# Optimization experiments

Measured on AMD Instinct MI355X. Metric: run time of the kernel, lower is better.

The kernel has to match this reference:

```python
import jax, jax.numpy as jnp
import numpy as np

B, P, D = 64, 1024, 768

def setup_inputs() -> dict:
    key = jax.random.key(0)
    k1, k2, k3 = jax.random.split(key, 3)
    z = jax.random.normal(k1, (B, P, D), dtype=jnp.float32)
    q = jax.random.normal(k2, (1, 1, D), dtype=jnp.float32)
    W_proj = jax.random.normal(k3, (D, D), dtype=jnp.float32) * (1.0 / np.sqrt(D))
    return {"z": z, "q": q, "W_proj": W_proj}

def reference(z, q, W_proj):
    # k = Linear(z) with weight W_proj (torch: z @ W.T), no bias
    k = jnp.einsum("bpd,ed->bpe", z, W_proj)          # [B,P,D]
    d = z.shape[-1]
    scale = 1.0 / jnp.sqrt(jnp.asarray(d, dtype=z.dtype))
    # single learnable query broadcast over batch: scores [B,1,P]
    scores = jnp.einsum("xqd,bpd->bqp", q, k) * scale
    attn = jax.nn.softmax(scores, axis=-1)            # [B,1,P]
    pooled = jnp.einsum("bqp,bpd->bqd", attn, z)      # [B,1,D]
    return pooled[:, 0, :]                            # [B,D]
```

## Files before the change

kernel.cpp:

```cpp
#include <hip/hip_runtime.h>
#include <math.h>

#define BB 64
#define PP 1024
#define DD 768
#define SS 8
#define TR 16
#define NT 8

__global__ __launch_bounds__(256) void qw_kernel(const float* __restrict__ q,
                                                 const float* __restrict__ W,
                                                 float* __restrict__ qw) {
    int d  = blockIdx.x * 256 + threadIdx.x;
    int e0 = blockIdx.y * 24;
    float acc = 0.f;
#pragma unroll
    for (int i = 0; i < 24; ++i) {
        int e = e0 + i;
        acc += q[e] * W[(size_t)e * DD + d];
    }
    atomicAdd(&qw[d], acc);
}

__global__ __launch_bounds__(256) void fused_kernel(const float* __restrict__ z,
                                                    const float* __restrict__ qw,
                                                    float* __restrict__ macc,
                                                    float* __restrict__ ml) {
    const float scale = 0.03608439182435161f;
    __shared__ float zt[TR * DD];
    __shared__ float qs[DD];
    __shared__ float sc[TR];

    int b     = blockIdx.x;
    int split = blockIdx.y;
    int tid   = threadIdx.x;

    for (int i = tid; i < DD; i += 256) qs[i] = qw[i];

    int row = tid >> 4;
    int l16 = tid & 15;

    float m = -INFINITY, l = 0.f;
    float a0 = 0.f, a1 = 0.f, a2 = 0.f;

    const float4* gz = (const float4*)(z + ((size_t)b * PP + split * 128) * DD);
    float4*       lz = (float4*)zt;
    const float4* q4 = (const float4*)qs;

    __syncthreads();

    for (int t = 0; t < NT; ++t) {
        float4 tmp[12];
#pragma unroll
        for (int k = 0; k < 12; ++k) tmp[k] = gz[(size_t)t * 3072 + k * 256 + tid];
#pragma unroll
        for (int k = 0; k < 12; ++k) lz[k * 256 + tid] = tmp[k];
        __syncthreads();

        float part = 0.f;
#pragma unroll
        for (int k = 0; k < 12; ++k) {
            float4 zv = lz[row * 192 + k * 16 + l16];
            float4 qv = q4[k * 16 + l16];
            part += zv.x * qv.x + zv.y * qv.y + zv.z * qv.z + zv.w * qv.w;
        }
#pragma unroll
        for (int mask = 8; mask >= 1; mask >>= 1)
            part += __shfl_xor(part, mask, 64);
        if (l16 == 0) sc[row] = part * scale;
        __syncthreads();

        float mt = sc[0];
#pragma unroll
        for (int r = 1; r < TR; ++r) mt = fmaxf(mt, sc[r]);
        float mn    = fmaxf(m, mt);
        float alpha = __expf(m - mn);
        m = mn;
        l *= alpha;
        a0 *= alpha; a1 *= alpha; a2 *= alpha;
#pragma unroll
        for (int r = 0; r < TR; ++r) {
            float e = __expf(sc[r] - mn);
            l  += e;
            a0 += e * zt[r * DD + tid];
            a1 += e * zt[r * DD + tid + 256];
            a2 += e * zt[r * DD + tid + 512];
        }
        __syncthreads();
    }

    int part_idx = b * SS + split;
    float* ap = macc + (size_t)part_idx * DD;
    ap[tid] = a0; ap[tid + 256] = a1; ap[tid + 512] = a2;
    if (tid == 0) { ml[part_idx * 2] = m; ml[part_idx * 2 + 1] = l; }
}

__global__ __launch_bounds__(256) void reduce_kernel(const float* __restrict__ macc,
                                                     const float* __restrict__ ml,
                                                     float* __restrict__ out) {
    int b   = blockIdx.x;
    int tid = threadIdx.x;

    float mk[SS], lk[SS];
#pragma unroll
    for (int k = 0; k < SS; ++k) {
        mk[k] = ml[(b * SS + k) * 2];
        lk[k] = ml[(b * SS + k) * 2 + 1];
    }
    float M = mk[0];
#pragma unroll
    for (int k = 1; k < SS; ++k) M = fmaxf(M, mk[k]);
    float L = 0.f, w[SS];
#pragma unroll
    for (int k = 0; k < SS; ++k) { w[k] = __expf(mk[k] - M); L += w[k] * lk[k]; }
    float inv = 1.f / L;

    const float* base = macc + (size_t)b * SS * DD;
#pragma unroll
    for (int j = 0; j < 3; ++j) {
        int d = j * 256 + tid;
        float acc = 0.f;
#pragma unroll
        for (int k = 0; k < SS; ++k) acc += w[k] * base[(size_t)k * DD + d];
        out[b * DD + d] = acc * inv;
    }
}

extern "C" void kernel_launch(void* const* d_in, const int* in_sizes, int n_in,
                              void* d_out, int out_size, void* d_ws, size_t ws_size,
                              hipStream_t stream) {
    const float* z = (const float*)d_in[0];
    const float* q = (const float*)d_in[1];
    const float* W = (const float*)d_in[2];
    float* out = (float*)d_out;

    char* ws = (char*)d_ws;
    float* qw   = (float*)ws;
    float* ml   = (float*)(ws + 4096);
    float* macc = (float*)(ws + 4096 + 8192);

    hipMemsetAsync(qw, 0, DD * sizeof(float), stream);
    dim3 qg(3, 32);
    qw_kernel<<<qg, 256, 0, stream>>>(q, W, qw);
    dim3 fg(BB, SS);
    fused_kernel<<<fg, 256, 0, stream>>>(z, qw, macc, ml);
    reduce_kernel<<<BB, 256, 0, stream>>>(macc, ml, out);
}
```

Baseline: 286.2 us.

## Stream z rows per wavefront with register prefetch and online softmax, double splits

Replaces the shared-memory tiled loop with per-wavefront row streaming. Each wave prefetches the next row into registers, computes the score with a full-wave shuffle reduction, and updates an online softmax accumulator. The four waves are merged in shared memory. Splits per batch go from 8 to 16, and the reduce kernel gains a grid dimension over D. This removes the block barriers and LDS round trips and raises parallelism, at the cost of a serial shuffle chain per row and limited loads in flight per wave.

Result: no change. 283.9 us (-0.8%).

```diff
diff --git a/kernel.cpp b/kernel.cpp
--- a/kernel.cpp
+++ b/kernel.cpp
@@ -4,18 +4,17 @@
 #define BB 64
 #define PP 1024
 #define DD 768
-#define SS 8
-#define TR 16
-#define NT 8
+#define SPLITS 16
+#define RPW (PP / SPLITS / 4)
 
 __global__ __launch_bounds__(256) void qw_kernel(const float* __restrict__ q,
                                                  const float* __restrict__ W,
                                                  float* __restrict__ qw) {
     int d  = blockIdx.x * 256 + threadIdx.x;
-    int e0 = blockIdx.y * 24;
+    int e0 = blockIdx.y * 12;
     float acc = 0.f;
 #pragma unroll
-    for (int i = 0; i < 24; ++i) {
+    for (int i = 0; i < 12; ++i) {
         int e = e0 + i;
         acc += q[e] * W[(size_t)e * DD + d];
     }
@@ -27,103 +26,108 @@
                                                     float* __restrict__ macc,
                                                     float* __restrict__ ml) {
     const float scale = 0.03608439182435161f;
-    __shared__ float zt[TR * DD];
-    __shared__ float qs[DD];
-    __shared__ float sc[TR];
-
     int b     = blockIdx.x;
     int split = blockIdx.y;
     int tid   = threadIdx.x;
+    int w     = tid >> 6;
+    int lane  = tid & 63;
 
-    for (int i = tid; i < DD; i += 256) qs[i] = qw[i];
+    const float4* q4 = (const float4*)qw;
+    float4 qf0 = q4[lane], qf1 = q4[lane + 64], qf2 = q4[lane + 128];
 
-    int row = tid >> 4;
-    int l16 = tid & 15;
+    const float4* rp = (const float4*)(z + ((size_t)b * PP + split * (PP / SPLITS)
+                                            + w * RPW) * DD);
 
     float m = -INFINITY, l = 0.f;
-    float a0 = 0.f, a1 = 0.f, a2 = 0.f;
+    float4 a0 = {0.f,0.f,0.f,0.f}, a1 = {0.f,0.f,0.f,0.f}, a2 = {0.f,0.f,0.f,0.f};
 
-    const float4* gz = (const float4*)(z + ((size_t)b * PP + split * 128) * DD);
-    float4*       lz = (float4*)zt;
-    const float4* q4 = (const float4*)qs;
+    float4 c0 = rp[lane], c1 = rp[lane + 64], c2 = rp[lane + 128];
 
+#pragma unroll
+    for (int r = 0; r < RPW; ++r) {
+        float4 n0 = c0, n1 = c1, n2 = c2;
+        if (r + 1 < RPW) {
+            const float4* np = rp + (size_t)(r + 1) * (DD / 4);
+            n0 = np[lane]; n1 = np[lane + 64]; n2 = np[lane + 128];
+        }
+
+        float part = c0.x*qf0.x + c0.y*qf0.y + c0.z*qf0.z + c0.w*qf0.w
+                   + c1.x*qf1.x + c1.y*qf1.y + c1.z*qf1.z + c1.w*qf1.w
+                   + c2.x*qf2.x + c2.y*qf2.y + c2.z*qf2.z + c2.w*qf2.w;
+#pragma unroll
+        for (int mask = 32; mask >= 1; mask >>= 1)
+            part += __shfl_xor(part, mask, 64);
+        float s = part * scale;
+
+        if (s > m) {
+            float alpha = __expf(m - s);
+            l *= alpha;
+            a0.x *= alpha; a0.y *= alpha; a0.z *= alpha; a0.w *= alpha;
+            a1.x *= alpha; a1.y *= alpha; a1.z *= alpha; a1.w *= alpha;
+            a2.x *= alpha; a2.y *= alpha; a2.z *= alpha; a2.w *= alpha;
+            m = s;
+        }
+        float e = __expf(s - m);
+        l += e;
+        a0.x += e * c0.x; a0.y += e * c0.y; a0.z += e * c0.z; a0.w += e * c0.w;
+        a1.x += e * c1.x; a1.y += e * c1.y; a1.z += e * c1.z; a1.w += e * c1.w;
+        a2.x += e * c2.x; a2.y += e * c2.y; a2.z += e * c2.z; a2.w += e * c2.w;
+
+        c0 = n0; c1 = n1; c2 = n2;
+    }
+
+    __shared__ float sacc[4][DD];
+    __shared__ float sml[4][2];
+    float4* sa = (float4*)sacc[w];
+    sa[lane] = a0; sa[lane + 64] = a1; sa[lane + 128] = a2;
+    if (lane == 0) { sml[w][0] = m; sml[w][1] = l; }
     __syncthreads();
 
-    for (int t = 0; t < NT; ++t) {
-        float4 tmp[12];
+    float M = fmaxf(fmaxf(sml[0][0], sml[1][0]), fmaxf(sml[2][0], sml[3][0]));
+    float wk[4], L = 0.f;
 #pragma unroll
-        for (int k = 0; k < 12; ++k) tmp[k] = gz[(size_t)t * 3072 + k * 256 + tid];
+    for (int k = 0; k < 4; ++k) { wk[k] = __expf(sml[k][0] - M); L += wk[k] * sml[k][1]; }
+
+    int pidx = b * SPLITS + split;
+    float* ap = macc + (size_t)pidx * DD;
 #pragma unroll
-        for (int k = 0; k < 12; ++k) lz[k * 256 + tid] = tmp[k];
-        __syncthreads();
-
-        float part = 0.f;
+    for (int j = 0; j < 3; ++j) {
+        int d = j * 256 + tid;
+        float acc = 0.f;
 #pragma unroll
-        for (int k = 0; k < 12; ++k) {
-            float4 zv = lz[row * 192 + k * 16 + l16];
-            float4 qv = q4[k * 16 + l16];
-            part += zv.x * qv.x + zv.y * qv.y + zv.z * qv.z + zv.w * qv.w;
-        }
-#pragma unroll
-        for (int mask = 8; mask >= 1; mask >>= 1)
-            part += __shfl_xor(part, mask, 64);
-        if (l16 == 0) sc[row] = part * scale;
-        __syncthreads();
-
-        float mt = sc[0];
-#pragma unroll
-        for (int r = 1; r < TR; ++r) mt = fmaxf(mt, sc[r]);
-        float mn    = fmaxf(m, mt);
-        float alpha = __expf(m - mn);
-        m = mn;
-        l *= alpha;
-        a0 *= alpha; a1 *= alpha; a2 *= alpha;
-#pragma unroll
-        for (int r = 0; r < TR; ++r) {
-            float e = __expf(sc[r] - mn);
-            l  += e;
-            a0 += e * zt[r * DD + tid];
-            a1 += e * zt[r * DD + tid + 256];
-            a2 += e * zt[r * DD + tid + 512];
-        }
-        __syncthreads();
+        for (int k = 0; k < 4; ++k) acc += wk[k] * sacc[k][d];
+        ap[d] = acc;
     }
-
-    int part_idx = b * SS + split;
-    float* ap = macc + (size_t)part_idx * DD;
-    ap[tid] = a0; ap[tid + 256] = a1; ap[tid + 512] = a2;
-    if (tid == 0) { ml[part_idx * 2] = m; ml[part_idx * 2 + 1] = l; }
+    if (tid == 0) { ml[pidx * 2] = M; ml[pidx * 2 + 1] = L; }
 }
 
 __global__ __launch_bounds__(256) void reduce_kernel(const float* __restrict__ macc,
                                                      const float* __restrict__ ml,
                                                      float* __restrict__ out) {
     int b   = blockIdx.x;
+    int j   = blockIdx.y;
     int tid = threadIdx.x;
 
-    float mk[SS], lk[SS];
+    float mk[SPLITS], lk[SPLITS];
 #pragma unroll
-    for (int k = 0; k < SS; ++k) {
-        mk[k] = ml[(b * SS + k) * 2];
-        lk[k] = ml[(b * SS + k) * 2 + 1];
+    for (int k = 0; k < SPLITS; ++k) {
+        mk[k] = ml[(b * SPLITS + k) * 2];
+        lk[k] = ml[(b * SPLITS + k) * 2 + 1];
     }
     float M = mk[0];
 #pragma unroll
-    for (int k = 1; k < SS; ++k) M = fmaxf(M, mk[k]);
-    float L = 0.f, w[SS];
+    for (int k = 1; k < SPLITS; ++k) M = fmaxf(M, mk[k]);
+    float L = 0.f, wk[SPLITS];
 #pragma unroll
-    for (int k = 0; k < SS; ++k) { w[k] = __expf(mk[k] - M); L += w[k] * lk[k]; }
+    for (int k = 0; k < SPLITS; ++k) { wk[k] = __expf(mk[k] - M); L += wk[k] * lk[k]; }
     float inv = 1.f / L;
 
-    const float* base = macc + (size_t)b * SS * DD;
+    int d = j * 256 + tid;
+    const float* base = macc + (size_t)b * SPLITS * DD;
+    float acc = 0.f;
 #pragma unroll
-    for (int j = 0; j < 3; ++j) {
-        int d = j * 256 + tid;
-        float acc = 0.f;
-#pragma unroll
-        for (int k = 0; k < SS; ++k) acc += w[k] * base[(size_t)k * DD + d];
-        out[b * DD + d] = acc * inv;
-    }
+    for (int k = 0; k < SPLITS; ++k) acc += wk[k] * base[(size_t)k * DD + d];
+    out[b * DD + d] = acc * inv;
 }
 
 extern "C" void kernel_launch(void* const* d_in, const int* in_sizes, int n_in,
@@ -140,9 +144,10 @@
     float* macc = (float*)(ws + 4096 + 8192);
 
     hipMemsetAsync(qw, 0, DD * sizeof(float), stream);
-    dim3 qg(3, 32);
+    dim3 qg(3, 64);
     qw_kernel<<<qg, 256, 0, stream>>>(q, W, qw);
-    dim3 fg(BB, SS);
+    dim3 fg(BB, SPLITS);
     fused_kernel<<<fg, 256, 0, stream>>>(z, qw, macc, ml);
-    reduce_kernel<<<BB, 256, 0, stream>>>(macc, ml, out);
+    dim3 rg(BB, 3);
+    reduce_kernel<<<rg, 256, 0, stream>>>(macc, ml, out);
 }
```
